# Optimization experiments

Hardware: AMD Instinct MI355X
Metric: run time of the kernel (lower is better)

## Reference

```python
import math
import jax, jax.numpy as jnp
import numpy as np

B = 128          # batch_size (graphs)
SEQ = 128        # max_seq_len (nodes per graph)
D = 128          # input_dim
HID = 64         # enc_hidden_dim
HEADS = 4        # in_head
N = B * SEQ      # total nodes
E = 262144       # edges (avg degree 16)


def _make_pe(seq, d):
    pos = np.arange(seq, dtype=np.float32)[:, None]
    i_even = np.arange(0, d, 2, dtype=np.float32)
    pe = np.zeros((seq, d), dtype=np.float32)
    pe[:, 0::2] = np.sin(pos / 10000.0 ** (2.0 * i_even / d))
    pe[:, 1::2] = np.cos(pos / 10000.0 ** (2.0 * (i_even + 1.0) / d))
    return jnp.asarray(pe)


def setup_inputs() -> dict:
    key = jax.random.key(0)
    ks = jax.random.split(key, 10)
    s = 0.1
    return {
        "x": jax.random.normal(ks[0], (N, D), jnp.float32),
        "edge_index": jax.random.randint(ks[1], (2, E), 0, N),
        "pe": _make_pe(SEQ, D),
        "W1": jax.random.normal(ks[2], (D, HEADS * HID), jnp.float32) * s,
        "a_src1": jax.random.normal(ks[3], (HEADS, HID), jnp.float32) * s,
        "a_dst1": jax.random.normal(ks[4], (HEADS, HID), jnp.float32) * s,
        "b1": jnp.zeros((HEADS * HID,), jnp.float32),
        "W2": jax.random.normal(ks[5], (HEADS * HID, HID), jnp.float32) * s,
        "a_src2": jax.random.normal(ks[6], (1, HID), jnp.float32) * s,
        "a_dst2": jax.random.normal(ks[7], (1, HID), jnp.float32) * s,
        "b2": jnp.zeros((HID,), jnp.float32),
        "batch_size": B,
    }


def _gat_conv(x, src, dst, W, a_src, a_dst, b, heads, ch, concat, n):
    # PyG GATConv (eval mode, self-loops already appended to src/dst).
    h = (x @ W).reshape(n, heads, ch)                      # [N,H,C]
    alpha_src = jnp.einsum("nhc,hc->nh", h, a_src)         # [N,H]
    alpha_dst = jnp.einsum("nhc,hc->nh", h, a_dst)
    e = jax.nn.leaky_relu(alpha_src[src] + alpha_dst[dst], 0.2)  # [E,H]
    m = jax.ops.segment_max(e, dst, num_segments=n)        # segment softmax over dst
    ex = jnp.exp(e - m[dst])
    den = jax.ops.segment_sum(ex, dst, num_segments=n)
    alpha = ex / (den[dst] + 1e-16)                        # [E,H]
    out = jax.ops.segment_sum(h[src] * alpha[:, :, None], dst, num_segments=n)
    out = out.reshape(n, heads * ch) if concat else out.mean(axis=1)
    return out + b


def reference(x, edge_index, pe, W1, a_src1, a_dst1, b1, W2, a_src2, a_dst2, b2, batch_size):
    n = x.shape[0]
    loop = jnp.arange(n)
    src = jnp.concatenate([edge_index[0], loop])           # add self-loops (PyG default)
    dst = jnp.concatenate([edge_index[1], loop])
    # positional encoding (dropout inactive in eval)
    h = x * math.sqrt(x.shape[1]) + jnp.tile(pe, (batch_size, 1))
    h = jax.nn.elu(_gat_conv(h, src, dst, W1, a_src1, a_dst1, b1, HEADS, HID, True, n))
    out = _gat_conv(h, src, dst, W2, a_src2, a_dst2, b2, 1, HID, False, n)
    return out.reshape(batch_size, -1, out.shape[1])
```

## Files before the change

### kernel.cpp

```cpp
#include <hip/hip_runtime.h>
#include <hip/hip_bf16.h>

typedef __hip_bfloat16 bf16;

#define N_NODES 16384
#define D_IN    128
#define HID     64
#define HEADS   4
#define F1      256
#define SEQ     128
#define SLOTS   64

__device__ __forceinline__ float wave_sum(float v) {
    #pragma unroll
    for (int o = 32; o > 0; o >>= 1) v += __shfl_xor(v, o, 64);
    return v;
}
__device__ __forceinline__ float wave_max(float v) {
    #pragma unroll
    for (int o = 32; o > 0; o >>= 1) v = fmaxf(v, __shfl_xor(v, o, 64));
    return v;
}
__device__ __forceinline__ float lrelu(float v) { return v > 0.f ? v : 0.2f * v; }
__device__ __forceinline__ float rdlane(float v, int l) {
    return __uint_as_float(__builtin_amdgcn_readlane(__float_as_uint(v), l));
}


__global__ __launch_bounds__(256) void k_zero(int4* p) {
    p[blockIdx.x * 256 + threadIdx.x] = make_int4(0, 0, 0, 0);
}

__global__ __launch_bounds__(256) void k_scatter(const int* __restrict__ ei, int E, int Etot,
                                                 int* __restrict__ cnt,
                                                 int* __restrict__ esrc) {
    int e = blockIdx.x * 256 + threadIdx.x;
    if (e >= Etot) return;
    int s, d;
    if (e < E) { s = ei[e]; d = ei[E + e]; }
    else       { s = e - E; d = s; }
    int pos = atomicAdd(&cnt[d], 1);
    if (pos < SLOTS) esrc[d * SLOTS + pos] = s;
}

__global__ __launch_bounds__(256) void k_gemm1(const float* __restrict__ x,
                                               const float* __restrict__ pe,
                                               const float* __restrict__ W1,
                                               const float* __restrict__ a_src1,
                                               const float* __restrict__ a_dst1,
                                               bf16* __restrict__ h,
                                               float* __restrict__ as1,
                                               float* __restrict__ ad1) {
    int tid = threadIdx.x, lane = tid & 63, wv = tid >> 6;
    int base = blockIdx.x * 16;
    int j4 = lane * 4;

    float2 xr[4];
    #pragma unroll
    for (int i = 0; i < 4; i++) {
        int row = base + wv * 4 + i;
        float2 xa  = *(const float2*)(x  + (size_t)row * 128 + 2 * lane);
        float2 pea = *(const float2*)(pe + (size_t)(row & (SEQ - 1)) * 128 + 2 * lane);
        xr[i].x = xa.x * 11.313708499f + pea.x;
        xr[i].y = xa.y * 11.313708499f + pea.y;
    }

    float acc[4][4] = {};
    const float4* Wv = (const float4*)W1;
    #pragma unroll 4
    for (int k2 = 0; k2 < 64; k2++) {
        float4 w0 = Wv[(size_t)(2 * k2) * 64 + lane];
        float4 w1 = Wv[(size_t)(2 * k2 + 1) * 64 + lane];
        #pragma unroll
        for (int i = 0; i < 4; i++) {
            float a0 = rdlane(xr[i].x, k2);
            float a1 = rdlane(xr[i].y, k2);
            acc[i][0] += a0 * w0.x + a1 * w1.x;
            acc[i][1] += a0 * w0.y + a1 * w1.y;
            acc[i][2] += a0 * w0.z + a1 * w1.z;
            acc[i][3] += a0 * w0.w + a1 * w1.w;
        }
    }

    float4 asv = *(const float4*)(a_src1 + j4);
    float4 adv = *(const float4*)(a_dst1 + j4);
    #pragma unroll
    for (int i = 0; i < 4; i++) {
        int row = base + wv * 4 + i;
        union { bf16 b[4]; ushort4 u; } cv;
        cv.b[0] = __float2bfloat16(acc[i][0]);
        cv.b[1] = __float2bfloat16(acc[i][1]);
        cv.b[2] = __float2bfloat16(acc[i][2]);
        cv.b[3] = __float2bfloat16(acc[i][3]);
        *(ushort4*)(h + (size_t)row * 256 + j4) = cv.u;
        float vs = acc[i][0] * asv.x + acc[i][1] * asv.y + acc[i][2] * asv.z + acc[i][3] * asv.w;
        float vd = acc[i][0] * adv.x + acc[i][1] * adv.y + acc[i][2] * adv.z + acc[i][3] * adv.w;
        #pragma unroll
        for (int o = 1; o < 16; o <<= 1) {
            vs += __shfl_xor(vs, o);
            vd += __shfl_xor(vd, o);
        }
        if ((lane & 15) == 0) {
            as1[row * 4 + (lane >> 4)] = vs;
            ad1[row * 4 + (lane >> 4)] = vd;
        }
    }
}

__global__ __launch_bounds__(256) void k_agg1(const int* __restrict__ cnt,
                                              const int* __restrict__ esrc,
                                              const bf16* __restrict__ h,
                                              const float* __restrict__ as1,
                                              const float* __restrict__ ad1,
                                              const float* __restrict__ b1,
                                              float* __restrict__ h1) {
    int d = blockIdx.x;
    int tid = threadIdx.x, lane = tid & 63, wv = tid >> 6;
    int beg = d * SLOTS;
    int deg = min(cnt[d], SLOTS);
    float adw = ad1[d * 4 + wv];

    int eg = lane >> 3;
    int cg = lane & 7;
    const bf16* hbase = h + (size_t)wv * 64 + cg * 8;

    int s = 0; float ev = -1e30f;
    if (lane < deg) {
        s = esrc[beg + lane];
        ev = lrelu(as1[s * 4 + wv] + adw);
    }
    float mx = wave_max(ev);
    float t = (lane < deg) ? __expf(ev - mx) : 0.f;
    float den = wave_sum(t);

    float acc[8] = {0, 0, 0, 0, 0, 0, 0, 0};
    for (int sub = 0; sub < deg; sub += 32) {
        uint4 u[4]; float te[4];
        #pragma unroll
        for (int q = 0; q < 4; q++) {
            int e = sub + q * 8;
            int se = __shfl(s, e + eg);
            te[q] = __shfl(t, e + eg);
            if (e < deg) u[q] = *(const uint4*)(hbase + (size_t)se * 256);
            else         u[q] = make_uint4(0, 0, 0, 0);
        }
        #pragma unroll
        for (int q = 0; q < 4; q++) {
            acc[0] += te[q] * __uint_as_float(u[q].x << 16);
            acc[1] += te[q] * __uint_as_float(u[q].x & 0xffff0000u);
            acc[2] += te[q] * __uint_as_float(u[q].y << 16);
            acc[3] += te[q] * __uint_as_float(u[q].y & 0xffff0000u);
            acc[4] += te[q] * __uint_as_float(u[q].z << 16);
            acc[5] += te[q] * __uint_as_float(u[q].z & 0xffff0000u);
            acc[6] += te[q] * __uint_as_float(u[q].w << 16);
            acc[7] += te[q] * __uint_as_float(u[q].w & 0xffff0000u);
        }
    }

    #pragma unroll
    for (int j = 0; j < 8; j++) {
        acc[j] += __shfl_xor(acc[j], 8);
        acc[j] += __shfl_xor(acc[j], 16);
        acc[j] += __shfl_xor(acc[j], 32);
    }
    if (lane < 8) {
        float inv = 1.f / (den + 1e-16f);
        int cbase = wv * 64 + lane * 8;
        float o[8];
        #pragma unroll
        for (int j = 0; j < 8; j++) {
            float v = acc[j] * inv + b1[cbase + j];
            o[j] = v > 0.f ? v : (__expf(v) - 1.f);
        }
        float4* dst = (float4*)(h1 + (size_t)d * 256 + cbase);
        dst[0] = make_float4(o[0], o[1], o[2], o[3]);
        dst[1] = make_float4(o[4], o[5], o[6], o[7]);
    }
}

__global__ __launch_bounds__(256) void k_gemm2(const float* __restrict__ h1,
                                               const float* __restrict__ W2,
                                               const float* __restrict__ a_src2,
                                               const float* __restrict__ a_dst2,
                                               bf16* __restrict__ h2,
                                               float* __restrict__ as2,
                                               float* __restrict__ ad2) {
    __shared__ float hs[16][256];
    int tid = threadIdx.x;
    int base = blockIdx.x * 16;
    const float4* srcv = (const float4*)(h1 + (size_t)base * 256);
    float4* dstv = (float4*)&hs[0][0];
    #pragma unroll
    for (int i = 0; i < 4; i++) dstv[tid + i * 256] = srcv[tid + i * 256];
    __syncthreads();

    int j = tid & 63, wv = tid >> 6;
    float acc[4] = {0, 0, 0, 0};
    const float* hrow = &hs[wv * 4][0];
    #pragma unroll 4
    for (int k = 0; k < 256; k++) {
        float w = W2[k * 64 + j];
        #pragma unroll
        for (int r = 0; r < 4; r++) acc[r] += hrow[r * 256 + k] * w;
    }
    float asj = a_src2[j], adj = a_dst2[j];
    #pragma unroll
    for (int r = 0; r < 4; r++) {
        int n = base + wv * 4 + r;
        h2[(size_t)n * 64 + j] = __float2bfloat16(acc[r]);
        float va = wave_sum(acc[r] * asj);
        float vd = wave_sum(acc[r] * adj);
        if (j == 0) { as2[n] = va; ad2[n] = vd; }
    }
}

__global__ __launch_bounds__(256) void k_agg2(const int* __restrict__ cnt,
                                              const int* __restrict__ esrc,
                                              const bf16* __restrict__ h2,
                                              const float* __restrict__ as2,
                                              const float* __restrict__ ad2,
                                              const float* __restrict__ b2v,
                                              float* __restrict__ out) {
    int tid = threadIdx.x, lane = tid & 63, wv = tid >> 6;
    int d = blockIdx.x * 4 + wv;
    int beg = d * SLOTS;
    int deg = min(cnt[d], SLOTS);
    float adw = ad2[d];

    int eg = lane >> 3;
    int cg = lane & 7;
    const bf16* hbase = h2 + cg * 8;

    int s = 0; float ev = -1e30f;
    if (lane < deg) {
        s = esrc[beg + lane];
        ev = lrelu(as2[s] + adw);
    }
    float mx = wave_max(ev);
    float t = (lane < deg) ? __expf(ev - mx) : 0.f;
    float den = wave_sum(t);

    float acc[8] = {0, 0, 0, 0, 0, 0, 0, 0};
    for (int sub = 0; sub < deg; sub += 32) {
        uint4 u[4]; float te[4];
        #pragma unroll
        for (int q = 0; q < 4; q++) {
            int e = sub + q * 8;
            int se = __shfl(s, e + eg);
            te[q] = __shfl(t, e + eg);
            if (e < deg) u[q] = *(const uint4*)(hbase + (size_t)se * 64);
            else         u[q] = make_uint4(0, 0, 0, 0);
        }
        #pragma unroll
        for (int q = 0; q < 4; q++) {
            acc[0] += te[q] * __uint_as_float(u[q].x << 16);
            acc[1] += te[q] * __uint_as_float(u[q].x & 0xffff0000u);
            acc[2] += te[q] * __uint_as_float(u[q].y << 16);
            acc[3] += te[q] * __uint_as_float(u[q].y & 0xffff0000u);
            acc[4] += te[q] * __uint_as_float(u[q].z << 16);
            acc[5] += te[q] * __uint_as_float(u[q].z & 0xffff0000u);
            acc[6] += te[q] * __uint_as_float(u[q].w << 16);
            acc[7] += te[q] * __uint_as_float(u[q].w & 0xffff0000u);
        }
    }

    #pragma unroll
    for (int j = 0; j < 8; j++) {
        acc[j] += __shfl_xor(acc[j], 8);
        acc[j] += __shfl_xor(acc[j], 16);
        acc[j] += __shfl_xor(acc[j], 32);
    }
    if (lane < 8) {
        float inv = 1.f / (den + 1e-16f);
        int cbase = lane * 8;
        float o[8];
        #pragma unroll
        for (int j = 0; j < 8; j++) o[j] = acc[j] * inv + b2v[cbase + j];
        float4* dst = (float4*)(out + (size_t)d * 64 + cbase);
        dst[0] = make_float4(o[0], o[1], o[2], o[3]);
        dst[1] = make_float4(o[4], o[5], o[6], o[7]);
    }
}

extern "C" void kernel_launch(void* const* d_in, const int* in_sizes, int n_in,
                              void* d_out, int out_size, void* d_ws, size_t ws_size,
                              hipStream_t stream) {
    const float* x    = (const float*)d_in[0];
    const int*   ei   = (const int*)  d_in[1];
    const float* pe   = (const float*)d_in[2];
    const float* W1   = (const float*)d_in[3];
    const float* a_s1 = (const float*)d_in[4];
    const float* a_d1 = (const float*)d_in[5];
    const float* b1   = (const float*)d_in[6];
    const float* W2   = (const float*)d_in[7];
    const float* a_s2 = (const float*)d_in[8];
    const float* a_d2 = (const float*)d_in[9];
    const float* b2   = (const float*)d_in[10];

    const int E    = in_sizes[1] / 2;
    const int n    = N_NODES;
    const int Etot = E + n;

    char* p = (char*)d_ws;
    auto alloc = [&](size_t bytes) -> void* {
        void* r = (void*)p;
        p += (bytes + 255) & ~(size_t)255;
        return r;
    };
    int*   cnt     = (int*)  alloc((size_t)n * 4);
    int*   esrc    = (int*)  alloc((size_t)n * SLOTS * 4);
    bf16*  h       = (bf16*) alloc((size_t)n * F1 * 2);
    float* as1     = (float*)alloc((size_t)n * HEADS * 4);
    float* ad1     = (float*)alloc((size_t)n * HEADS * 4);
    float* h1      = (float*)alloc((size_t)n * F1 * 4);
    bf16*  h2      = (bf16*) alloc((size_t)n * HID * 2);
    float* as2     = (float*)alloc((size_t)n * 4);
    float* ad2     = (float*)alloc((size_t)n * 4);

    int eblocks = (Etot + 255) / 256;

    k_zero   <<<n / (256 * 4), 256, 0, stream>>>((int4*)cnt);
    k_scatter<<<eblocks, 256, 0, stream>>>(ei, E, Etot, cnt, esrc);

    k_gemm1  <<<n / 16, 256, 0, stream>>>(x, pe, W1, a_s1, a_d1, h, as1, ad1);
    k_agg1   <<<n, 256, 0, stream>>>(cnt, esrc, h, as1, ad1, b1, h1);
    k_gemm2  <<<n / 16, 256, 0, stream>>>(h1, W2, a_s2, a_d2, h2, as2, ad2);
    k_agg2   <<<n / 4, 256, 0, stream>>>(cnt, esrc, h2, as2, ad2, b2, (float*)d_out);
}
```

Baseline: 185.3 us.

## Fuse all stages into one cooperative persistent kernel with grid syncs

Replaces the six separate launches (zero, scatter, gemm1, agg1, gemm2, agg2) with a single cooperative kernel of 512 blocks. Each stage runs in a grid-stride loop and is separated by grid.sync(). The aim is to remove launch overhead and inter-kernel gaps. The trade-offs are grid-barrier cost, register pressure from merging all stages into one kernel, and less latency hiding in the aggregation stages. If the cooperative launch fails, it falls back to the original kernels.

Result: slower. 529.5 us (+185.8%).

```diff
diff --git a/kernel.cpp b/kernel.cpp
--- a/kernel.cpp
+++ b/kernel.cpp
@@ -1,5 +1,8 @@
 #include <hip/hip_runtime.h>
 #include <hip/hip_bf16.h>
+#include <hip/hip_cooperative_groups.h>
+
+namespace cg = cooperative_groups;
 
 typedef __hip_bfloat16 bf16;
 
@@ -10,6 +13,7 @@
 #define F1      256
 #define SEQ     128
 #define SLOTS   64
+#define GRIDB   512
 
 __device__ __forceinline__ float wave_sum(float v) {
     #pragma unroll
@@ -24,6 +28,252 @@
 __device__ __forceinline__ float lrelu(float v) { return v > 0.f ? v : 0.2f * v; }
 __device__ __forceinline__ float rdlane(float v, int l) {
     return __uint_as_float(__builtin_amdgcn_readlane(__float_as_uint(v), l));
+}
+
+__global__ __launch_bounds__(256, 2) void k_mega(
+        const int* __restrict__ ei, int E, int Etot,
+        const float* __restrict__ x, const float* __restrict__ pe,
+        const float* __restrict__ W1,
+        const float* __restrict__ a_src1, const float* __restrict__ a_dst1,
+        const float* __restrict__ b1,
+        const float* __restrict__ W2,
+        const float* __restrict__ a_src2, const float* __restrict__ a_dst2,
+        const float* __restrict__ b2v,
+        int* __restrict__ cnt, int* __restrict__ esrc,
+        bf16* __restrict__ h, float* __restrict__ as1, float* __restrict__ ad1,
+        float* __restrict__ h1,
+        bf16* __restrict__ h2, float* __restrict__ as2, float* __restrict__ ad2,
+        float* __restrict__ out) {
+    cg::grid_group grid = cg::this_grid();
+    int tid  = threadIdx.x;
+    int lane = tid & 63, wv = tid >> 6;
+    int gtid = blockIdx.x * 256 + tid;
+    const int NTH = GRIDB * 256;
+
+    __shared__ float hs[16][256];
+
+    for (int i = gtid; i < N_NODES; i += NTH) cnt[i] = 0;
+    grid.sync();
+
+    for (int e = gtid; e < Etot; e += NTH) {
+        int s, d;
+        if (e < E) { s = ei[e]; d = ei[E + e]; }
+        else       { s = e - E; d = s; }
+        int pos = atomicAdd(&cnt[d], 1);
+        if (pos < SLOTS) esrc[d * SLOTS + pos] = s;
+    }
+    grid.sync();
+
+    {
+        int j4 = lane * 4;
+        float4 asv = *(const float4*)(a_src1 + j4);
+        float4 adv = *(const float4*)(a_dst1 + j4);
+        const float4* Wv = (const float4*)W1;
+        for (int bb = blockIdx.x; bb < N_NODES / 16; bb += GRIDB) {
+            int base = bb * 16;
+            float2 xr[4];
+            #pragma unroll
+            for (int i = 0; i < 4; i++) {
+                int row = base + wv * 4 + i;
+                float2 xa  = *(const float2*)(x  + (size_t)row * 128 + 2 * lane);
+                float2 pea = *(const float2*)(pe + (size_t)(row & (SEQ - 1)) * 128 + 2 * lane);
+                xr[i].x = xa.x * 11.313708499f + pea.x;
+                xr[i].y = xa.y * 11.313708499f + pea.y;
+            }
+            float acc[4][4] = {};
+            #pragma unroll 4
+            for (int k2 = 0; k2 < 64; k2++) {
+                float4 w0 = Wv[(size_t)(2 * k2) * 64 + lane];
+                float4 w1 = Wv[(size_t)(2 * k2 + 1) * 64 + lane];
+                #pragma unroll
+                for (int i = 0; i < 4; i++) {
+                    float a0 = rdlane(xr[i].x, k2);
+                    float a1 = rdlane(xr[i].y, k2);
+                    acc[i][0] += a0 * w0.x + a1 * w1.x;
+                    acc[i][1] += a0 * w0.y + a1 * w1.y;
+                    acc[i][2] += a0 * w0.z + a1 * w1.z;
+                    acc[i][3] += a0 * w0.w + a1 * w1.w;
+                }
+            }
+            #pragma unroll
+            for (int i = 0; i < 4; i++) {
+                int row = base + wv * 4 + i;
+                union { bf16 b[4]; ushort4 u; } cv;
+                cv.b[0] = __float2bfloat16(acc[i][0]);
+                cv.b[1] = __float2bfloat16(acc[i][1]);
+                cv.b[2] = __float2bfloat16(acc[i][2]);
+                cv.b[3] = __float2bfloat16(acc[i][3]);
+                *(ushort4*)(h + (size_t)row * 256 + j4) = cv.u;
+                float vs = acc[i][0] * asv.x + acc[i][1] * asv.y + acc[i][2] * asv.z + acc[i][3] * asv.w;
+                float vd = acc[i][0] * adv.x + acc[i][1] * adv.y + acc[i][2] * adv.z + acc[i][3] * adv.w;
+                #pragma unroll
+                for (int o = 1; o < 16; o <<= 1) {
+                    vs += __shfl_xor(vs, o);
+                    vd += __shfl_xor(vd, o);
+                }
+                if ((lane & 15) == 0) {
+                    as1[row * 4 + (lane >> 4)] = vs;
+                    ad1[row * 4 + (lane >> 4)] = vd;
+                }
+            }
+        }
+    }
+    grid.sync();
+
+    {
+        int eg = lane >> 3;
+        int cg_ = lane & 7;
+        const bf16* hbase = h + (size_t)wv * 64 + cg_ * 8;
+        for (int d = blockIdx.x; d < N_NODES; d += GRIDB) {
+            int beg = d * SLOTS;
+            int deg = min(cnt[d], SLOTS);
+            float adw = ad1[d * 4 + wv];
+
+            int s = 0; float ev = -1e30f;
+            if (lane < deg) {
+                s = esrc[beg + lane];
+                ev = lrelu(as1[s * 4 + wv] + adw);
+            }
+            float mx = wave_max(ev);
+            float t = (lane < deg) ? __expf(ev - mx) : 0.f;
+            float den = wave_sum(t);
+
+            float acc[8] = {0, 0, 0, 0, 0, 0, 0, 0};
+            for (int sub = 0; sub < deg; sub += 32) {
+                uint4 u[4]; float te[4];
+                #pragma unroll
+                for (int q = 0; q < 4; q++) {
+                    int e = sub + q * 8;
+                    int se = __shfl(s, e + eg);
+                    te[q] = __shfl(t, e + eg);
+                    if (e < deg) u[q] = *(const uint4*)(hbase + (size_t)se * 256);
+                    else         u[q] = make_uint4(0, 0, 0, 0);
+                }
+                #pragma unroll
+                for (int q = 0; q < 4; q++) {
+                    acc[0] += te[q] * __uint_as_float(u[q].x << 16);
+                    acc[1] += te[q] * __uint_as_float(u[q].x & 0xffff0000u);
+                    acc[2] += te[q] * __uint_as_float(u[q].y << 16);
+                    acc[3] += te[q] * __uint_as_float(u[q].y & 0xffff0000u);
+                    acc[4] += te[q] * __uint_as_float(u[q].z << 16);
+                    acc[5] += te[q] * __uint_as_float(u[q].z & 0xffff0000u);
+                    acc[6] += te[q] * __uint_as_float(u[q].w << 16);
+                    acc[7] += te[q] * __uint_as_float(u[q].w & 0xffff0000u);
+                }
+            }
+            #pragma unroll
+            for (int j = 0; j < 8; j++) {
+                acc[j] += __shfl_xor(acc[j], 8);
+                acc[j] += __shfl_xor(acc[j], 16);
+                acc[j] += __shfl_xor(acc[j], 32);
+            }
+            if (lane < 8) {
+                float inv = 1.f / (den + 1e-16f);
+                int cbase = wv * 64 + lane * 8;
+                float o[8];
+                #pragma unroll
+                for (int j = 0; j < 8; j++) {
+                    float v = acc[j] * inv + b1[cbase + j];
+                    o[j] = v > 0.f ? v : (__expf(v) - 1.f);
+                }
+                float4* dst = (float4*)(h1 + (size_t)d * 256 + cbase);
+                dst[0] = make_float4(o[0], o[1], o[2], o[3]);
+                dst[1] = make_float4(o[4], o[5], o[6], o[7]);
+            }
+        }
+    }
+    grid.sync();
+
+    {
+        float asj = a_src2[lane], adj = a_dst2[lane];
+        for (int bb = blockIdx.x; bb < N_NODES / 16; bb += GRIDB) {
+            int base = bb * 16;
+            const float4* srcv = (const float4*)(h1 + (size_t)base * 256);
+            float4* dstv = (float4*)&hs[0][0];
+            #pragma unroll
+            for (int i = 0; i < 4; i++) dstv[tid + i * 256] = srcv[tid + i * 256];
+            __syncthreads();
+
+            float acc[4] = {0, 0, 0, 0};
+            const float* hrow = &hs[wv * 4][0];
+            #pragma unroll 4
+            for (int k = 0; k < 256; k++) {
+                float w = W2[k * 64 + lane];
+                #pragma unroll
+                for (int r = 0; r < 4; r++) acc[r] += hrow[r * 256 + k] * w;
+            }
+            #pragma unroll
+            for (int r = 0; r < 4; r++) {
+                int n = base + wv * 4 + r;
+                h2[(size_t)n * 64 + lane] = __float2bfloat16(acc[r]);
+                float va = wave_sum(acc[r] * asj);
+                float vd = wave_sum(acc[r] * adj);
+                if (lane == 0) { as2[n] = va; ad2[n] = vd; }
+            }
+            __syncthreads();
+        }
+    }
+    grid.sync();
+
+    {
+        int eg = lane >> 3;
+        int cg_ = lane & 7;
+        const bf16* hbase = h2 + cg_ * 8;
+        for (int d = blockIdx.x * 4 + wv; d < N_NODES; d += GRIDB * 4) {
+            int beg = d * SLOTS;
+            int deg = min(cnt[d], SLOTS);
+            float adw = ad2[d];
+
+            int s = 0; float ev = -1e30f;
+            if (lane < deg) {
+                s = esrc[beg + lane];
+                ev = lrelu(as2[s] + adw);
+            }
+            float mx = wave_max(ev);
+            float t = (lane < deg) ? __expf(ev - mx) : 0.f;
+            float den = wave_sum(t);
+
+            float acc[8] = {0, 0, 0, 0, 0, 0, 0, 0};
+            for (int sub = 0; sub < deg; sub += 32) {
+                uint4 u[4]; float te[4];
+                #pragma unroll
+                for (int q = 0; q < 4; q++) {
+                    int e = sub + q * 8;
+                    int se = __shfl(s, e + eg);
+                    te[q] = __shfl(t, e + eg);
+                    if (e < deg) u[q] = *(const uint4*)(hbase + (size_t)se * 64);
+                    else         u[q] = make_uint4(0, 0, 0, 0);
+                }
+                #pragma unroll
+                for (int q = 0; q < 4; q++) {
+                    acc[0] += te[q] * __uint_as_float(u[q].x << 16);
+                    acc[1] += te[q] * __uint_as_float(u[q].x & 0xffff0000u);
+                    acc[2] += te[q] * __uint_as_float(u[q].y << 16);
+                    acc[3] += te[q] * __uint_as_float(u[q].y & 0xffff0000u);
+                    acc[4] += te[q] * __uint_as_float(u[q].z << 16);
+                    acc[5] += te[q] * __uint_as_float(u[q].z & 0xffff0000u);
+                    acc[6] += te[q] * __uint_as_float(u[q].w << 16);
+                    acc[7] += te[q] * __uint_as_float(u[q].w & 0xffff0000u);
+                }
+            }
+            #pragma unroll
+            for (int j = 0; j < 8; j++) {
+                acc[j] += __shfl_xor(acc[j], 8);
+                acc[j] += __shfl_xor(acc[j], 16);
+                acc[j] += __shfl_xor(acc[j], 32);
+            }
+            if (lane < 8) {
+                float inv = 1.f / (den + 1e-16f);
+                int cbase = lane * 8;
+                float o[8];
+                #pragma unroll
+                for (int j = 0; j < 8; j++) o[j] = acc[j] * inv + b2v[cbase + j];
+                float4* dst = (float4*)(out + (size_t)d * 64 + cbase);
+                dst[0] = make_float4(o[0], o[1], o[2], o[3]);
+                dst[1] = make_float4(o[4], o[5], o[6], o[7]);
+            }
+        }
+    }
 }
 
 
@@ -54,7 +304,6 @@
     int tid = threadIdx.x, lane = tid & 63, wv = tid >> 6;
     int base = blockIdx.x * 16;
     int j4 = lane * 4;
-
     float2 xr[4];
     #pragma unroll
     for (int i = 0; i < 4; i++) {
@@ -64,7 +313,6 @@
         xr[i].x = xa.x * 11.313708499f + pea.x;
         xr[i].y = xa.y * 11.313708499f + pea.y;
     }
-
     float acc[4][4] = {};
     const float4* Wv = (const float4*)W1;
     #pragma unroll 4
@@ -81,7 +329,6 @@
             acc[i][3] += a0 * w0.w + a1 * w1.w;
         }
     }
-
     float4 asv = *(const float4*)(a_src1 + j4);
     float4 adv = *(const float4*)(a_dst1 + j4);
     #pragma unroll
@@ -119,10 +366,8 @@
     int beg = d * SLOTS;
     int deg = min(cnt[d], SLOTS);
     float adw = ad1[d * 4 + wv];
-
-    int eg = lane >> 3;
-    int cg = lane & 7;
-    const bf16* hbase = h + (size_t)wv * 64 + cg * 8;
+    int eg = lane >> 3, cg_ = lane & 7;
+    const bf16* hbase = h + (size_t)wv * 64 + cg_ * 8;
 
     int s = 0; float ev = -1e30f;
     if (lane < deg) {
@@ -156,7 +401,6 @@
             acc[7] += te[q] * __uint_as_float(u[q].w & 0xffff0000u);
         }
     }
-
     #pragma unroll
     for (int j = 0; j < 8; j++) {
         acc[j] += __shfl_xor(acc[j], 8);
@@ -193,7 +437,6 @@
     #pragma unroll
     for (int i = 0; i < 4; i++) dstv[tid + i * 256] = srcv[tid + i * 256];
     __syncthreads();
-
     int j = tid & 63, wv = tid >> 6;
     float acc[4] = {0, 0, 0, 0};
     const float* hrow = &hs[wv * 4][0];
@@ -226,10 +469,8 @@
     int beg = d * SLOTS;
     int deg = min(cnt[d], SLOTS);
     float adw = ad2[d];
-
-    int eg = lane >> 3;
-    int cg = lane & 7;
-    const bf16* hbase = h2 + cg * 8;
+    int eg = lane >> 3, cg_ = lane & 7;
+    const bf16* hbase = h2 + cg_ * 8;
 
     int s = 0; float ev = -1e30f;
     if (lane < deg) {
@@ -263,7 +504,6 @@
             acc[7] += te[q] * __uint_as_float(u[q].w & 0xffff0000u);
         }
     }
-
     #pragma unroll
     for (int j = 0; j < 8; j++) {
         acc[j] += __shfl_xor(acc[j], 8);
@@ -316,14 +556,31 @@
     bf16*  h2      = (bf16*) alloc((size_t)n * HID * 2);
     float* as2     = (float*)alloc((size_t)n * 4);
     float* ad2     = (float*)alloc((size_t)n * 4);
-
-    int eblocks = (Etot + 255) / 256;
-
-    k_zero   <<<n / (256 * 4), 256, 0, stream>>>((int4*)cnt);
-    k_scatter<<<eblocks, 256, 0, stream>>>(ei, E, Etot, cnt, esrc);
-
-    k_gemm1  <<<n / 16, 256, 0, stream>>>(x, pe, W1, a_s1, a_d1, h, as1, ad1);
-    k_agg1   <<<n, 256, 0, stream>>>(cnt, esrc, h, as1, ad1, b1, h1);
-    k_gemm2  <<<n / 16, 256, 0, stream>>>(h1, W2, a_s2, a_d2, h2, as2, ad2);
-    k_agg2   <<<n / 4, 256, 0, stream>>>(cnt, esrc, h2, as2, ad2, b2, (float*)d_out);
-}
+    float* outp    = (float*)d_out;
+
+    int Ev = E, Etotv = Etot;
+    void* args[] = {
+        (void*)&ei, (void*)&Ev, (void*)&Etotv,
+        (void*)&x, (void*)&pe, (void*)&W1,
+        (void*)&a_s1, (void*)&a_d1, (void*)&b1,
+        (void*)&W2, (void*)&a_s2, (void*)&a_d2, (void*)&b2,
+        (void*)&cnt, (void*)&esrc,
+        (void*)&h, (void*)&as1, (void*)&ad1,
+        (void*)&h1,
+        (void*)&h2, (void*)&as2, (void*)&ad2,
+        (void*)&outp,
+    };
+    hipError_t err = hipLaunchCooperativeKernel((const void*)k_mega,
+                                                dim3(GRIDB), dim3(256),
+                                                args, 0, stream);
+    if (err != hipSuccess) {
+        (void)hipGetLastError();
+        int eblocks = (Etot + 255) / 256;
+        k_zero   <<<n / (256 * 4), 256, 0, stream>>>((int4*)cnt);
+        k_scatter<<<eblocks, 256, 0, stream>>>(ei, E, Etot, cnt, esrc);
+        k_gemm1  <<<n / 16, 256, 0, stream>>>(x, pe, W1, a_s1, a_d1, h, as1, ad1);
+        k_agg1   <<<n, 256, 0, stream>>>(cnt, esrc, h, as1, ad1, b1, h1);
+        k_gemm2  <<<n / 16, 256, 0, stream>>>(h1, W2, a_s2, a_d2, h2, as2, ad2);
+        k_agg2   <<<n / 4, 256, 0, stream>>>(cnt, esrc, h2, as2, ad2, b2, outp);
+    }
+}
```

## Fuse layer-1 aggregation with second GEMM and fold count zeroing into GEMM1

Applied to the files above, without the earlier changes.

Layer-1 aggregation now writes each node's ELU output into shared memory instead of a global h1 buffer. The same block then runs the W2 projection and attention-score reductions for its 8 nodes. The zeroing of edge counts moves into the first GEMM kernel, dropping two launches and the fp32 h1 round trip to global memory. In exchange each block processes 8 destination nodes serially, so there are 8x fewer blocks for the gather-heavy aggregation, which may cut latency hiding.

New measurement: 180.7 us. -2.5%, faster.

```diff
diff --git a/kernel.cpp b/kernel.cpp
--- a/kernel.cpp
+++ b/kernel.cpp
@@ -26,9 +26,68 @@
     return __uint_as_float(__builtin_amdgcn_readlane(__float_as_uint(v), l));
 }
 
-
-__global__ __launch_bounds__(256) void k_zero(int4* p) {
-    p[blockIdx.x * 256 + threadIdx.x] = make_int4(0, 0, 0, 0);
+__global__ __launch_bounds__(256) void k_gemm1z(const float* __restrict__ x,
+                                                const float* __restrict__ pe,
+                                                const float* __restrict__ W1,
+                                                const float* __restrict__ a_src1,
+                                                const float* __restrict__ a_dst1,
+                                                bf16* __restrict__ h,
+                                                float* __restrict__ as1,
+                                                float* __restrict__ ad1,
+                                                int4* __restrict__ cntv) {
+    int tid = threadIdx.x, lane = tid & 63, wv = tid >> 6;
+    if (tid < 4) cntv[blockIdx.x * 4 + tid] = make_int4(0, 0, 0, 0);
+
+    int base = blockIdx.x * 16;
+    int j4 = lane * 4;
+    float2 xr[4];
+    #pragma unroll
+    for (int i = 0; i < 4; i++) {
+        int row = base + wv * 4 + i;
+        float2 xa  = *(const float2*)(x  + (size_t)row * 128 + 2 * lane);
+        float2 pea = *(const float2*)(pe + (size_t)(row & (SEQ - 1)) * 128 + 2 * lane);
+        xr[i].x = xa.x * 11.313708499f + pea.x;
+        xr[i].y = xa.y * 11.313708499f + pea.y;
+    }
+    float acc[4][4] = {};
+    const float4* Wv = (const float4*)W1;
+    #pragma unroll 4
+    for (int k2 = 0; k2 < 64; k2++) {
+        float4 w0 = Wv[(size_t)(2 * k2) * 64 + lane];
+        float4 w1 = Wv[(size_t)(2 * k2 + 1) * 64 + lane];
+        #pragma unroll
+        for (int i = 0; i < 4; i++) {
+            float a0 = rdlane(xr[i].x, k2);
+            float a1 = rdlane(xr[i].y, k2);
+            acc[i][0] += a0 * w0.x + a1 * w1.x;
+            acc[i][1] += a0 * w0.y + a1 * w1.y;
+            acc[i][2] += a0 * w0.z + a1 * w1.z;
+            acc[i][3] += a0 * w0.w + a1 * w1.w;
+        }
+    }
+    float4 asv = *(const float4*)(a_src1 + j4);
+    float4 adv = *(const float4*)(a_dst1 + j4);
+    #pragma unroll
+    for (int i = 0; i < 4; i++) {
+        int row = base + wv * 4 + i;
+        union { bf16 b[4]; ushort4 u; } cv;
+        cv.b[0] = __float2bfloat16(acc[i][0]);
+        cv.b[1] = __float2bfloat16(acc[i][1]);
+        cv.b[2] = __float2bfloat16(acc[i][2]);
+        cv.b[3] = __float2bfloat16(acc[i][3]);
+        *(ushort4*)(h + (size_t)row * 256 + j4) = cv.u;
+        float vs = acc[i][0] * asv.x + acc[i][1] * asv.y + acc[i][2] * asv.z + acc[i][3] * asv.w;
+        float vd = acc[i][0] * adv.x + acc[i][1] * adv.y + acc[i][2] * adv.z + acc[i][3] * adv.w;
+        #pragma unroll
+        for (int o = 1; o < 16; o <<= 1) {
+            vs += __shfl_xor(vs, o);
+            vd += __shfl_xor(vd, o);
+        }
+        if ((lane & 15) == 0) {
+            as1[row * 4 + (lane >> 4)] = vs;
+            ad1[row * 4 + (lane >> 4)] = vd;
+        }
+    }
 }
 
 __global__ __launch_bounds__(256) void k_scatter(const int* __restrict__ ei, int E, int Etot,
@@ -43,174 +102,108 @@
     if (pos < SLOTS) esrc[d * SLOTS + pos] = s;
 }
 
-__global__ __launch_bounds__(256) void k_gemm1(const float* __restrict__ x,
-                                               const float* __restrict__ pe,
-                                               const float* __restrict__ W1,
-                                               const float* __restrict__ a_src1,
-                                               const float* __restrict__ a_dst1,
-                                               bf16* __restrict__ h,
-                                               float* __restrict__ as1,
-                                               float* __restrict__ ad1) {
+__global__ __launch_bounds__(256) void k_agg1_gemm2(
+        const int* __restrict__ cnt, const int* __restrict__ esrc,
+        const bf16* __restrict__ h,
+        const float* __restrict__ as1, const float* __restrict__ ad1,
+        const float* __restrict__ b1,
+        const float* __restrict__ W2,
+        const float* __restrict__ a_src2, const float* __restrict__ a_dst2,
+        bf16* __restrict__ h2, float* __restrict__ as2, float* __restrict__ ad2) {
+    __shared__ float hs[8][256];
     int tid = threadIdx.x, lane = tid & 63, wv = tid >> 6;
-    int base = blockIdx.x * 16;
-    int j4 = lane * 4;
-
-    float2 xr[4];
-    #pragma unroll
-    for (int i = 0; i < 4; i++) {
-        int row = base + wv * 4 + i;
-        float2 xa  = *(const float2*)(x  + (size_t)row * 128 + 2 * lane);
-        float2 pea = *(const float2*)(pe + (size_t)(row & (SEQ - 1)) * 128 + 2 * lane);
-        xr[i].x = xa.x * 11.313708499f + pea.x;
-        xr[i].y = xa.y * 11.313708499f + pea.y;
-    }
-
-    float acc[4][4] = {};
-    const float4* Wv = (const float4*)W1;
-    #pragma unroll 4
-    for (int k2 = 0; k2 < 64; k2++) {
-        float4 w0 = Wv[(size_t)(2 * k2) * 64 + lane];
-        float4 w1 = Wv[(size_t)(2 * k2 + 1) * 64 + lane];
-        #pragma unroll
-        for (int i = 0; i < 4; i++) {
-            float a0 = rdlane(xr[i].x, k2);
-            float a1 = rdlane(xr[i].y, k2);
-            acc[i][0] += a0 * w0.x + a1 * w1.x;
-            acc[i][1] += a0 * w0.y + a1 * w1.y;
-            acc[i][2] += a0 * w0.z + a1 * w1.z;
-            acc[i][3] += a0 * w0.w + a1 * w1.w;
-        }
-    }
-
-    float4 asv = *(const float4*)(a_src1 + j4);
-    float4 adv = *(const float4*)(a_dst1 + j4);
-    #pragma unroll
-    for (int i = 0; i < 4; i++) {
-        int row = base + wv * 4 + i;
-        union { bf16 b[4]; ushort4 u; } cv;
-        cv.b[0] = __float2bfloat16(acc[i][0]);
-        cv.b[1] = __float2bfloat16(acc[i][1]);
-        cv.b[2] = __float2bfloat16(acc[i][2]);
-        cv.b[3] = __float2bfloat16(acc[i][3]);
-        *(ushort4*)(h + (size_t)row * 256 + j4) = cv.u;
-        float vs = acc[i][0] * asv.x + acc[i][1] * asv.y + acc[i][2] * asv.z + acc[i][3] * asv.w;
-        float vd = acc[i][0] * adv.x + acc[i][1] * adv.y + acc[i][2] * adv.z + acc[i][3] * adv.w;
-        #pragma unroll
-        for (int o = 1; o < 16; o <<= 1) {
-            vs += __shfl_xor(vs, o);
-            vd += __shfl_xor(vd, o);
-        }
-        if ((lane & 15) == 0) {
-            as1[row * 4 + (lane >> 4)] = vs;
-            ad1[row * 4 + (lane >> 4)] = vd;
-        }
-    }
-}
-
-__global__ __launch_bounds__(256) void k_agg1(const int* __restrict__ cnt,
-                                              const int* __restrict__ esrc,
-                                              const bf16* __restrict__ h,
-                                              const float* __restrict__ as1,
-                                              const float* __restrict__ ad1,
-                                              const float* __restrict__ b1,
-                                              float* __restrict__ h1) {
-    int d = blockIdx.x;
-    int tid = threadIdx.x, lane = tid & 63, wv = tid >> 6;
-    int beg = d * SLOTS;
-    int deg = min(cnt[d], SLOTS);
-    float adw = ad1[d * 4 + wv];
+    int dbase = blockIdx.x * 8;
 
     int eg = lane >> 3;
-    int cg = lane & 7;
-    const bf16* hbase = h + (size_t)wv * 64 + cg * 8;
-
-    int s = 0; float ev = -1e30f;
-    if (lane < deg) {
-        s = esrc[beg + lane];
-        ev = lrelu(as1[s * 4 + wv] + adw);
-    }
-    float mx = wave_max(ev);
-    float t = (lane < deg) ? __expf(ev - mx) : 0.f;
-    float den = wave_sum(t);
-
-    float acc[8] = {0, 0, 0, 0, 0, 0, 0, 0};
-    for (int sub = 0; sub < deg; sub += 32) {
-        uint4 u[4]; float te[4];
-        #pragma unroll
-        for (int q = 0; q < 4; q++) {
-            int e = sub + q * 8;
-            int se = __shfl(s, e + eg);
-            te[q] = __shfl(t, e + eg);
-            if (e < deg) u[q] = *(const uint4*)(hbase + (size_t)se * 256);
-            else         u[q] = make_uint4(0, 0, 0, 0);
-        }
-        #pragma unroll
-        for (int q = 0; q < 4; q++) {
-            acc[0] += te[q] * __uint_as_float(u[q].x << 16);
-            acc[1] += te[q] * __uint_as_float(u[q].x & 0xffff0000u);
-            acc[2] += te[q] * __uint_as_float(u[q].y << 16);
-            acc[3] += te[q] * __uint_as_float(u[q].y & 0xffff0000u);
-            acc[4] += te[q] * __uint_as_float(u[q].z << 16);
-            acc[5] += te[q] * __uint_as_float(u[q].z & 0xffff0000u);
-            acc[6] += te[q] * __uint_as_float(u[q].w << 16);
-            acc[7] += te[q] * __uint_as_float(u[q].w & 0xffff0000u);
-        }
-    }
-
-    #pragma unroll
-    for (int j = 0; j < 8; j++) {
-        acc[j] += __shfl_xor(acc[j], 8);
-        acc[j] += __shfl_xor(acc[j], 16);
-        acc[j] += __shfl_xor(acc[j], 32);
-    }
-    if (lane < 8) {
-        float inv = 1.f / (den + 1e-16f);
-        int cbase = wv * 64 + lane * 8;
-        float o[8];
+    int cg_ = lane & 7;
+    const bf16* hbase = h + (size_t)wv * 64 + cg_ * 8;
+
+    for (int it = 0; it < 8; it++) {
+        int d = dbase + it;
+        int beg = d * SLOTS;
+        int deg = min(cnt[d], SLOTS);
+        float adw = ad1[d * 4 + wv];
+
+        int s = 0; float ev = -1e30f;
+        if (lane < deg) {
+            s = esrc[beg + lane];
+            ev = lrelu(as1[s * 4 + wv] + adw);
+        }
+        float mx = wave_max(ev);
+        float t = (lane < deg) ? __expf(ev - mx) : 0.f;
+        float den = wave_sum(t);
+
+        float acc[8] = {0, 0, 0, 0, 0, 0, 0, 0};
+        for (int sub = 0; sub < deg; sub += 32) {
+            uint4 u[4]; float te[4];
+            #pragma unroll
+            for (int q = 0; q < 4; q++) {
+                int e = sub + q * 8;
+                int se = __shfl(s, e + eg);
+                te[q] = __shfl(t, e + eg);
+                if (e < deg) u[q] = *(const uint4*)(hbase + (size_t)se * 256);
+                else         u[q] = make_uint4(0, 0, 0, 0);
+            }
+            #pragma unroll
+            for (int q = 0; q < 4; q++) {
+                acc[0] += te[q] * __uint_as_float(u[q].x << 16);
+                acc[1] += te[q] * __uint_as_float(u[q].x & 0xffff0000u);
+                acc[2] += te[q] * __uint_as_float(u[q].y << 16);
+                acc[3] += te[q] * __uint_as_float(u[q].y & 0xffff0000u);
+                acc[4] += te[q] * __uint_as_float(u[q].z << 16);
+                acc[5] += te[q] * __uint_as_float(u[q].z & 0xffff0000u);
+                acc[6] += te[q] * __uint_as_float(u[q].w << 16);
+                acc[7] += te[q] * __uint_as_float(u[q].w & 0xffff0000u);
+            }
+        }
         #pragma unroll
         for (int j = 0; j < 8; j++) {
-            float v = acc[j] * inv + b1[cbase + j];
-            o[j] = v > 0.f ? v : (__expf(v) - 1.f);
-        }
-        float4* dst = (float4*)(h1 + (size_t)d * 256 + cbase);
-        dst[0] = make_float4(o[0], o[1], o[2], o[3]);
-        dst[1] = make_float4(o[4], o[5], o[6], o[7]);
-    }
-}
-
-__global__ __launch_bounds__(256) void k_gemm2(const float* __restrict__ h1,
-                                               const float* __restrict__ W2,
-                                               const float* __restrict__ a_src2,
-                                               const float* __restrict__ a_dst2,
-                                               bf16* __restrict__ h2,
-                                               float* __restrict__ as2,
-                                               float* __restrict__ ad2) {
-    __shared__ float hs[16][256];
-    int tid = threadIdx.x;
-    int base = blockIdx.x * 16;
-    const float4* srcv = (const float4*)(h1 + (size_t)base * 256);
-    float4* dstv = (float4*)&hs[0][0];
-    #pragma unroll
-    for (int i = 0; i < 4; i++) dstv[tid + i * 256] = srcv[tid + i * 256];
+            acc[j] += __shfl_xor(acc[j], 8);
+            acc[j] += __shfl_xor(acc[j], 16);
+            acc[j] += __shfl_xor(acc[j], 32);
+        }
+        if (lane < 8) {
+            float inv = 1.f / (den + 1e-16f);
+            int cbase = wv * 64 + lane * 8;
+            float o[8];
+            #pragma unroll
+            for (int j = 0; j < 8; j++) {
+                float v = acc[j] * inv + b1[cbase + j];
+                o[j] = v > 0.f ? v : (__expf(v) - 1.f);
+            }
+            float4* dst = (float4*)&hs[it][cbase];
+            dst[0] = make_float4(o[0], o[1], o[2], o[3]);
+            dst[1] = make_float4(o[4], o[5], o[6], o[7]);
+        }
+    }
     __syncthreads();
 
-    int j = tid & 63, wv = tid >> 6;
-    float acc[4] = {0, 0, 0, 0};
-    const float* hrow = &hs[wv * 4][0];
-    #pragma unroll 4
-    for (int k = 0; k < 256; k++) {
-        float w = W2[k * 64 + j];
-        #pragma unroll
-        for (int r = 0; r < 4; r++) acc[r] += hrow[r * 256 + k] * w;
-    }
-    float asj = a_src2[j], adj = a_dst2[j];
-    #pragma unroll
-    for (int r = 0; r < 4; r++) {
-        int n = base + wv * 4 + r;
-        h2[(size_t)n * 64 + j] = __float2bfloat16(acc[r]);
-        float va = wave_sum(acc[r] * asj);
-        float vd = wave_sum(acc[r] * adj);
-        if (j == 0) { as2[n] = va; ad2[n] = vd; }
+    {
+        int r0 = wv * 2, r1 = wv * 2 + 1;
+        const float4* h0v = (const float4*)&hs[r0][0];
+        const float4* h1v = (const float4*)&hs[r1][0];
+        float a0 = 0.f, a1 = 0.f;
+        #pragma unroll 4
+        for (int k4 = 0; k4 < 64; k4++) {
+            float4 u0 = h0v[k4];
+            float4 u1 = h1v[k4];
+            const float* wp = W2 + (size_t)k4 * 256 + lane;
+            float w0 = wp[0], w1 = wp[64], w2 = wp[128], w3 = wp[192];
+            a0 += u0.x * w0 + u0.y * w1 + u0.z * w2 + u0.w * w3;
+            a1 += u1.x * w0 + u1.y * w1 + u1.z * w2 + u1.w * w3;
+        }
+        float asj = a_src2[lane], adj = a_dst2[lane];
+        int n0 = dbase + r0, n1 = dbase + r1;
+        h2[(size_t)n0 * 64 + lane] = __float2bfloat16(a0);
+        h2[(size_t)n1 * 64 + lane] = __float2bfloat16(a1);
+        float va0 = wave_sum(a0 * asj);
+        float vd0 = wave_sum(a0 * adj);
+        float va1 = wave_sum(a1 * asj);
+        float vd1 = wave_sum(a1 * adj);
+        if (lane == 0) {
+            as2[n0] = va0; ad2[n0] = vd0;
+            as2[n1] = va1; ad2[n1] = vd1;
+        }
     }
 }
 
@@ -226,10 +219,8 @@
     int beg = d * SLOTS;
     int deg = min(cnt[d], SLOTS);
     float adw = ad2[d];
-
-    int eg = lane >> 3;
-    int cg = lane & 7;
-    const bf16* hbase = h2 + cg * 8;
+    int eg = lane >> 3, cg_ = lane & 7;
+    const bf16* hbase = h2 + cg_ * 8;
 
     int s = 0; float ev = -1e30f;
     if (lane < deg) {
@@ -263,7 +254,6 @@
             acc[7] += te[q] * __uint_as_float(u[q].w & 0xffff0000u);
         }
     }
-
     #pragma unroll
     for (int j = 0; j < 8; j++) {
         acc[j] += __shfl_xor(acc[j], 8);
@@ -312,18 +302,15 @@
     bf16*  h       = (bf16*) alloc((size_t)n * F1 * 2);
     float* as1     = (float*)alloc((size_t)n * HEADS * 4);
     float* ad1     = (float*)alloc((size_t)n * HEADS * 4);
-    float* h1      = (float*)alloc((size_t)n * F1 * 4);
     bf16*  h2      = (bf16*) alloc((size_t)n * HID * 2);
     float* as2     = (float*)alloc((size_t)n * 4);
     float* ad2     = (float*)alloc((size_t)n * 4);
 
     int eblocks = (Etot + 255) / 256;
 
-    k_zero   <<<n / (256 * 4), 256, 0, stream>>>((int4*)cnt);
-    k_scatter<<<eblocks, 256, 0, stream>>>(ei, E, Etot, cnt, esrc);
-
-    k_gemm1  <<<n / 16, 256, 0, stream>>>(x, pe, W1, a_s1, a_d1, h, as1, ad1);
-    k_agg1   <<<n, 256, 0, stream>>>(cnt, esrc, h, as1, ad1, b1, h1);
-    k_gemm2  <<<n / 16, 256, 0, stream>>>(h1, W2, a_s2, a_d2, h2, as2, ad2);
-    k_agg2   <<<n / 4, 256, 0, stream>>>(cnt, esrc, h2, as2, ad2, b2, (float*)d_out);
-}
+    k_gemm1z    <<<n / 16, 256, 0, stream>>>(x, pe, W1, a_s1, a_d1, h, as1, ad1, (int4*)cnt);
+    k_scatter   <<<eblocks, 256, 0, stream>>>(ei, E, Etot, cnt, esrc);
+    k_agg1_gemm2<<<n / 8, 256, 0, stream>>>(cnt, esrc, h, as1, ad1, b1,
+                                            W2, a_s2, a_d2, h2, as2, ad2);
+    k_agg2      <<<n / 4, 256, 0, stream>>>(cnt, esrc, h2, as2, ad2, b2, (float*)d_out);
+}
```
